# Optimization experiments

Measured on AMD Instinct MI355X. Metric: run time of the kernel, lower is better.

The kernel has to match this reference:

```python
import jax, jax.numpy as jnp
import numpy as np

N_NODES = 50000
N_EDGES = 800000
IN_DIM = 128
HID_DIM = 128
LAT_DIM = 64
NEG_SLOPE = 0.01


def _leaky(v):
    return jnp.where(v >= 0, v, NEG_SLOPE * v)


def _gcn_conv(x, W, b, src, dst, n_nodes):
    # PyG GCNConv: h = x @ W; add self-loops; sym-normalized sum aggregation; + bias
    h = x @ W  # [N, out]
    ones = jnp.ones(src.shape[0], h.dtype)
    deg = jax.ops.segment_sum(ones, dst, num_segments=n_nodes) + 1.0  # +1 self-loop
    dinv = jax.lax.rsqrt(deg)  # deg >= 1 so always finite
    norm = dinv[src] * dinv[dst]  # [E]
    agg = jax.ops.segment_sum(h[src] * norm[:, None], dst, num_segments=n_nodes)
    agg = agg + h * (dinv * dinv)[:, None]  # self-loop term: norm_ii = 1/deg_i
    return agg + b


def _glorot(key, fan_in, fan_out):
    s = jnp.sqrt(6.0 / (fan_in + fan_out)).astype(jnp.float32)
    return jax.random.uniform(key, (fan_in, fan_out), jnp.float32, -s, s)


def setup_inputs() -> dict:
    key = jax.random.key(0)
    ks = jax.random.split(key, 10)
    x = jax.random.normal(ks[0], (N_NODES, IN_DIM), jnp.float32)
    edge_index = jax.random.randint(ks[1], (2, N_EDGES), 0, N_NODES, jnp.int64)
    return {
        "x": x,
        "edge_index": edge_index,
        "W1": _glorot(ks[2], IN_DIM, HID_DIM), "b1": jnp.zeros((HID_DIM,), jnp.float32),
        "W2": _glorot(ks[3], HID_DIM, HID_DIM), "b2": jnp.zeros((HID_DIM,), jnp.float32),
        "W3": _glorot(ks[4], HID_DIM, HID_DIM), "b3": jnp.zeros((HID_DIM,), jnp.float32),
        "W4": _glorot(ks[5], HID_DIM, LAT_DIM), "b4": jnp.zeros((LAT_DIM,), jnp.float32),
        "W5": _glorot(ks[6], LAT_DIM, HID_DIM), "b5": jnp.zeros((HID_DIM,), jnp.float32),
        "Wd": _glorot(ks[7], HID_DIM, IN_DIM), "bd": jnp.zeros((IN_DIM,), jnp.float32),
    }


def reference(x, edge_index, W1, b1, W2, b2, W3, b3, W4, b4, W5, b5, Wd, bd):
    src, dst = edge_index[0], edge_index[1]
    n = x.shape[0]
    # dropout is eval-mode identity
    x1 = _leaky(_gcn_conv(x, W1, b1, src, dst, n))
    x2 = _leaky(_gcn_conv(x1, W2, b2, src, dst, n))
    x3 = _leaky(_gcn_conv(x2, W3, b3, src, dst, n)) + x2  # residual
    z = _gcn_conv(x3, W4, b4, src, dst, n)
    xr = _leaky(_gcn_conv(z, W5, b5, src, dst, n))
    reconstructed = xr @ Wd + bd + x
    return (reconstructed, z)
```

## Files before the change

### kernel.cpp

```cpp
#include <hip/hip_runtime.h>
#include <hip/hip_fp16.h>

#define NEG_SLOPE 0.01f

typedef __attribute__((ext_vector_type(4))) _Float16 half4v;
typedef __attribute__((ext_vector_type(8))) _Float16 half8v;
typedef __attribute__((ext_vector_type(4))) float f32x4;


__global__ __launch_bounds__(256) void k_count(const int* __restrict__ dst,
                                               int* __restrict__ cnt, int E) {
  int e = blockIdx.x * 256 + threadIdx.x;
  if (e < E) atomicAdd(&cnt[dst[e]], 1);
}

__global__ __launch_bounds__(256) void k_dinv(const int* __restrict__ cnt,
                                              float* __restrict__ dinv, int n) {
  int i = blockIdx.x * 256 + threadIdx.x;
  if (i < n) dinv[i] = rsqrtf((float)cnt[i] + 1.0f);
}

__global__ __launch_bounds__(256) void k_scan1(const int* __restrict__ cnt,
                                               int* __restrict__ local,
                                               int* __restrict__ bsum, int n) {
  __shared__ int lds[256];
  int b = blockIdx.x, t = threadIdx.x;
  int base = b * 1024 + t * 4;
  int v0 = (base + 0 < n) ? cnt[base + 0] : 0;
  int v1 = (base + 1 < n) ? cnt[base + 1] : 0;
  int v2 = (base + 2 < n) ? cnt[base + 2] : 0;
  int v3 = (base + 3 < n) ? cnt[base + 3] : 0;
  int s = v0 + v1 + v2 + v3;
  lds[t] = s;
  __syncthreads();
  for (int ofs = 1; ofs < 256; ofs <<= 1) {
    int x = (t >= ofs) ? lds[t - ofs] : 0;
    __syncthreads();
    lds[t] += x;
    __syncthreads();
  }
  int run = lds[t] - s;
  run += v0; if (base + 0 < n) local[base + 0] = run;
  run += v1; if (base + 1 < n) local[base + 1] = run;
  run += v2; if (base + 2 < n) local[base + 2] = run;
  run += v3; if (base + 3 < n) local[base + 3] = run;
  if (t == 255) bsum[b] = lds[255];
}

__global__ __launch_bounds__(64) void k_scan2(const int* __restrict__ bsum,
                                              int* __restrict__ bofs, int nb) {
  __shared__ int lds[64];
  int t = threadIdx.x;
  int v = (t < nb) ? bsum[t] : 0;
  lds[t] = v;
  __syncthreads();
  for (int ofs = 1; ofs < 64; ofs <<= 1) {
    int x = (t >= ofs) ? lds[t - ofs] : 0;
    __syncthreads();
    lds[t] += x;
    __syncthreads();
  }
  if (t < nb) bofs[t] = lds[t] - v;
}

__global__ __launch_bounds__(256) void k_scan3(const int* __restrict__ local,
                                               const int* __restrict__ bofs,
                                               int* __restrict__ rowptr, int n) {
  int i = blockIdx.x * 256 + threadIdx.x;
  if (i < n) rowptr[i + 1] = local[i] + bofs[i >> 10];
  if (i == 0) rowptr[0] = 0;
}

__global__ __launch_bounds__(256) void k_fill(const int* __restrict__ src,
                                              const int* __restrict__ dst,
                                              const int* __restrict__ rowptr,
                                              int* __restrict__ cursor,
                                              int2* __restrict__ slots,
                                              const float* __restrict__ dinv, int E) {
  int e = blockIdx.x * 256 + threadIdx.x;
  if (e < E) {
    int s = src[e], d = dst[e];
    int p = rowptr[d] + atomicAdd(&cursor[d], 1);
    slots[p] = make_int2(s, __float_as_int(dinv[s] * dinv[d]));
  }
}

__global__ __launch_bounds__(256) void k_wt(const float* __restrict__ W,
                                            _Float16* __restrict__ Wt, int K, int M) {
  int i = blockIdx.x * 256 + threadIdx.x;
  if (i < K * M) {
    int k = i / M, m = i % M;
    Wt[(size_t)m * K + k] = (_Float16)W[(size_t)k * M + m];
  }
}

template <int NJ>
__global__ __launch_bounds__(256) void k_hgemm(const float* __restrict__ A,
                                               const _Float16* __restrict__ Bt,
                                               float* __restrict__ C,
                                               __half* __restrict__ C16, int N, int K,
                                               int M, const float* __restrict__ bias,
                                               int leaky,
                                               const float* __restrict__ addp) {
  __shared__ _Float16 Ah[64][40];
  __shared__ _Float16 Al[64][40];
  __shared__ _Float16 Bs[NJ * 32][40];
  int t = threadIdx.x;
  int row0 = blockIdx.x * 64;
  int lane = t & 63;
  int wid = t >> 6;
  int wr = wid >> 1, wc = wid & 1;
  int l15 = lane & 15, lg = lane >> 4;
  f32x4 acc[2][NJ] = {};
  for (int k0 = 0; k0 < K; k0 += 32) {
    __syncthreads();
    for (int i = t; i < 512; i += 256) {
      int r = i >> 3, kq = i & 7;
      int gr = row0 + r;
      float4 v = make_float4(0.f, 0.f, 0.f, 0.f);
      if (gr < N) v = *(const float4*)&A[(size_t)gr * K + k0 + kq * 4];
      half4v hi = {(_Float16)v.x, (_Float16)v.y, (_Float16)v.z, (_Float16)v.w};
      half4v lo = {(_Float16)(v.x - (float)hi[0]), (_Float16)(v.y - (float)hi[1]),
                   (_Float16)(v.z - (float)hi[2]), (_Float16)(v.w - (float)hi[3])};
      *(half4v*)&Ah[r][kq * 4] = hi;
      *(half4v*)&Al[r][kq * 4] = lo;
    }
    for (int i = t; i < NJ * 32 * 4; i += 256) {
      int c = i >> 2, kg = i & 3;
      *(half8v*)&Bs[c][kg * 8] = *(const half8v*)&Bt[(size_t)c * K + k0 + kg * 8];
    }
    __syncthreads();
    half8v ah0 = *(half8v*)&Ah[wr * 32 + l15][lg * 8];
    half8v ah1 = *(half8v*)&Ah[wr * 32 + 16 + l15][lg * 8];
    half8v al0 = *(half8v*)&Al[wr * 32 + l15][lg * 8];
    half8v al1 = *(half8v*)&Al[wr * 32 + 16 + l15][lg * 8];
#pragma unroll
    for (int nj = 0; nj < NJ; ++nj) {
      half8v bf = *(half8v*)&Bs[wc * (NJ * 16) + nj * 16 + l15][lg * 8];
      acc[0][nj] = __builtin_amdgcn_mfma_f32_16x16x32_f16(ah0, bf, acc[0][nj], 0, 0, 0);
      acc[0][nj] = __builtin_amdgcn_mfma_f32_16x16x32_f16(al0, bf, acc[0][nj], 0, 0, 0);
      acc[1][nj] = __builtin_amdgcn_mfma_f32_16x16x32_f16(ah1, bf, acc[1][nj], 0, 0, 0);
      acc[1][nj] = __builtin_amdgcn_mfma_f32_16x16x32_f16(al1, bf, acc[1][nj], 0, 0, 0);
    }
  }
#pragma unroll
  for (int mi = 0; mi < 2; ++mi) {
#pragma unroll
    for (int nj = 0; nj < NJ; ++nj) {
      int c = wc * (NJ * 16) + nj * 16 + l15;
#pragma unroll
      for (int jj = 0; jj < 4; ++jj) {
        int r = row0 + wr * 32 + mi * 16 + lg * 4 + jj;
        if (r >= N) continue;
        float v = acc[mi][nj][jj];
        if (bias) v += bias[c];
        if (leaky) v = (v >= 0.f) ? v : NEG_SLOPE * v;
        if (addp) v += addp[(size_t)r * M + c];
        if (C16) C16[(size_t)r * M + c] = __float2half(v);
        else C[(size_t)r * M + c] = v;
      }
    }
  }
}

__global__ __launch_bounds__(256) void k_agg128(const __half* __restrict__ h,
                                                const int* __restrict__ rowptr,
                                                const int2* __restrict__ slots,
                                                const float* __restrict__ dinv,
                                                const float* __restrict__ bias,
                                                const float* __restrict__ resid,
                                                float* __restrict__ out, int n,
                                                int leaky) {
  int w = (blockIdx.x * 256 + threadIdx.x) >> 6;
  int lane = threadIdx.x & 63;
  if (w >= n) return;
  int beg = rowptr[w], end = rowptr[w + 1];
  float a0 = 0.f, a1 = 0.f, c0 = 0.f, c1 = 0.f;
  int j = beg;
  for (; j + 8 <= end; j += 8) {
    int2 e0 = slots[j + 0], e1 = slots[j + 1], e2 = slots[j + 2], e3 = slots[j + 3];
    int2 e4 = slots[j + 4], e5 = slots[j + 5], e6 = slots[j + 6], e7 = slots[j + 7];
    float2 h0 = __half22float2(*(const __half2*)&h[(size_t)e0.x * 128 + lane * 2]);
    float2 h1 = __half22float2(*(const __half2*)&h[(size_t)e1.x * 128 + lane * 2]);
    float2 h2 = __half22float2(*(const __half2*)&h[(size_t)e2.x * 128 + lane * 2]);
    float2 h3 = __half22float2(*(const __half2*)&h[(size_t)e3.x * 128 + lane * 2]);
    float2 h4 = __half22float2(*(const __half2*)&h[(size_t)e4.x * 128 + lane * 2]);
    float2 h5 = __half22float2(*(const __half2*)&h[(size_t)e5.x * 128 + lane * 2]);
    float2 h6 = __half22float2(*(const __half2*)&h[(size_t)e6.x * 128 + lane * 2]);
    float2 h7 = __half22float2(*(const __half2*)&h[(size_t)e7.x * 128 + lane * 2]);
    float w0 = __int_as_float(e0.y), w1 = __int_as_float(e1.y);
    float w2 = __int_as_float(e2.y), w3 = __int_as_float(e3.y);
    float w4 = __int_as_float(e4.y), w5 = __int_as_float(e5.y);
    float w6 = __int_as_float(e6.y), w7 = __int_as_float(e7.y);
    a0 += w0 * h0.x; a1 += w0 * h0.y;
    c0 += w1 * h1.x; c1 += w1 * h1.y;
    a0 += w2 * h2.x; a1 += w2 * h2.y;
    c0 += w3 * h3.x; c1 += w3 * h3.y;
    a0 += w4 * h4.x; a1 += w4 * h4.y;
    c0 += w5 * h5.x; c1 += w5 * h5.y;
    a0 += w6 * h6.x; a1 += w6 * h6.y;
    c0 += w7 * h7.x; c1 += w7 * h7.y;
  }
  for (; j < end; ++j) {
    int2 ee = slots[j];
    float wt = __int_as_float(ee.y);
    float2 hv = __half22float2(*(const __half2*)&h[(size_t)ee.x * 128 + lane * 2]);
    a0 += wt * hv.x;
    a1 += wt * hv.y;
  }
  a0 += c0; a1 += c1;
  float di = dinv[w];
  float sw = di * di;
  float2 hs = __half22float2(*(const __half2*)&h[(size_t)w * 128 + lane * 2]);
  a0 += sw * hs.x;
  a1 += sw * hs.y;
  if (bias) {
    a0 += bias[lane * 2];
    a1 += bias[lane * 2 + 1];
  }
  if (leaky) {
    a0 = (a0 >= 0.f) ? a0 : NEG_SLOPE * a0;
    a1 = (a1 >= 0.f) ? a1 : NEG_SLOPE * a1;
  }
  if (resid) {
    float2 rv = *(const float2*)&resid[(size_t)w * 128 + lane * 2];
    a0 += rv.x;
    a1 += rv.y;
  }
  *(float2*)&out[(size_t)w * 128 + lane * 2] = make_float2(a0, a1);
}

__global__ __launch_bounds__(256) void k_agg64(const __half* __restrict__ h,
                                               const int* __restrict__ rowptr,
                                               const int2* __restrict__ slots,
                                               const float* __restrict__ dinv,
                                               const float* __restrict__ bias,
                                               float* __restrict__ out,
                                               __half* __restrict__ out16, int n,
                                               int leaky) {
  int w = (blockIdx.x * 256 + threadIdx.x) >> 6;
  int lane = threadIdx.x & 63;
  if (w >= n) return;
  int beg = rowptr[w], end = rowptr[w + 1];
  float a0 = 0.f, c0 = 0.f;
  int j = beg;
  for (; j + 8 <= end; j += 8) {
    int2 e0 = slots[j + 0], e1 = slots[j + 1], e2 = slots[j + 2], e3 = slots[j + 3];
    int2 e4 = slots[j + 4], e5 = slots[j + 5], e6 = slots[j + 6], e7 = slots[j + 7];
    float h0 = __half2float(h[(size_t)e0.x * 64 + lane]);
    float h1 = __half2float(h[(size_t)e1.x * 64 + lane]);
    float h2 = __half2float(h[(size_t)e2.x * 64 + lane]);
    float h3 = __half2float(h[(size_t)e3.x * 64 + lane]);
    float h4 = __half2float(h[(size_t)e4.x * 64 + lane]);
    float h5 = __half2float(h[(size_t)e5.x * 64 + lane]);
    float h6 = __half2float(h[(size_t)e6.x * 64 + lane]);
    float h7 = __half2float(h[(size_t)e7.x * 64 + lane]);
    a0 += __int_as_float(e0.y) * h0;
    c0 += __int_as_float(e1.y) * h1;
    a0 += __int_as_float(e2.y) * h2;
    c0 += __int_as_float(e3.y) * h3;
    a0 += __int_as_float(e4.y) * h4;
    c0 += __int_as_float(e5.y) * h5;
    a0 += __int_as_float(e6.y) * h6;
    c0 += __int_as_float(e7.y) * h7;
  }
  for (; j < end; ++j) {
    int2 ee = slots[j];
    a0 += __int_as_float(ee.y) * __half2float(h[(size_t)ee.x * 64 + lane]);
  }
  a0 += c0;
  float di = dinv[w];
  a0 += di * di * __half2float(h[(size_t)w * 64 + lane]);
  if (bias) a0 += bias[lane];
  if (leaky) a0 = (a0 >= 0.f) ? a0 : NEG_SLOPE * a0;
  out[(size_t)w * 64 + lane] = a0;
  if (out16) out16[(size_t)w * 64 + lane] = __float2half(a0);
}


extern "C" void kernel_launch(void* const* d_in, const int* in_sizes, int n_in,
                              void* d_out, int out_size, void* d_ws, size_t ws_size,
                              hipStream_t stream) {
  const float* x   = (const float*)d_in[0];
  const int* eidx  = (const int*)d_in[1];
  const float* W1  = (const float*)d_in[2];
  const float* b1  = (const float*)d_in[3];
  const float* W2  = (const float*)d_in[4];
  const float* b2  = (const float*)d_in[5];
  const float* W3  = (const float*)d_in[6];
  const float* b3  = (const float*)d_in[7];
  const float* W4  = (const float*)d_in[8];
  const float* b4  = (const float*)d_in[9];
  const float* W5  = (const float*)d_in[10];
  const float* b5  = (const float*)d_in[11];
  const float* Wd  = (const float*)d_in[12];
  const float* bd  = (const float*)d_in[13];

  const int N = in_sizes[0] / 128;
  const int E = in_sizes[1] / 2;
  const int* srcA = eidx;
  const int* dstA = eidx + E;

  char* ws = (char*)d_ws;
  size_t off = 0;
  auto carve = [&](size_t bytes) {
    char* p = ws + off;
    off = (off + bytes + 255) & ~(size_t)255;
    return p;
  };
  int*   cnt      = (int*)carve((size_t)N * 4);
  int*   rowptr   = (int*)carve((size_t)(N + 1) * 4);
  int*   cursor   = (int*)carve((size_t)N * 4);
  int*   local    = (int*)carve((size_t)N * 4);
  int*   bsum     = (int*)carve(64 * 4);
  int*   bofs     = (int*)carve(64 * 4);
  float* dinv     = (float*)carve((size_t)N * 4);
  int2*  slots    = (int2*)carve((size_t)E * 8);
  float* bufA     = (float*)carve((size_t)N * 128 * 4);
  float* bufB     = (float*)carve((size_t)N * 128 * 4);
  float* bufC     = (float*)carve((size_t)N * 128 * 4);
  _Float16* Wt1   = (_Float16*)carve(128 * 128 * 2);
  _Float16* Wt2   = (_Float16*)carve(128 * 128 * 2);
  _Float16* Wt3   = (_Float16*)carve(128 * 128 * 2);
  _Float16* Wt4   = (_Float16*)carve(128 * 64 * 2);
  _Float16* Wt5   = (_Float16*)carve(64 * 128 * 2);
  _Float16* Wtd   = (_Float16*)carve(128 * 128 * 2);

  __half* h16 = (__half*)bufA;
  __half* z16 = (__half*)((char*)bufA + (size_t)N * 256);

  float* recon = (float*)d_out;
  float* zout  = (float*)d_out + (size_t)N * 128;

  const int nb = (N + 1023) / 1024;
  dim3 b256(256);

  hipMemsetAsync(cnt, 0, (size_t)N * 4, stream);
  hipMemsetAsync(cursor, 0, (size_t)N * 4, stream);
  k_count<<<(E + 255) / 256, b256, 0, stream>>>(dstA, cnt, E);
  k_dinv<<<(N + 255) / 256, b256, 0, stream>>>(cnt, dinv, N);
  k_scan1<<<nb, b256, 0, stream>>>(cnt, local, bsum, N);
  k_scan2<<<1, 64, 0, stream>>>(bsum, bofs, nb);
  k_scan3<<<(N + 255) / 256, b256, 0, stream>>>(local, bofs, rowptr, N);
  k_fill<<<(E + 255) / 256, b256, 0, stream>>>(srcA, dstA, rowptr, cursor, slots,
                                               dinv, E);

  k_wt<<<(128 * 128 + 255) / 256, b256, 0, stream>>>(W1, Wt1, 128, 128);
  k_wt<<<(128 * 128 + 255) / 256, b256, 0, stream>>>(W2, Wt2, 128, 128);
  k_wt<<<(128 * 128 + 255) / 256, b256, 0, stream>>>(W3, Wt3, 128, 128);
  k_wt<<<(128 * 64 + 255) / 256, b256, 0, stream>>>(W4, Wt4, 128, 64);
  k_wt<<<(64 * 128 + 255) / 256, b256, 0, stream>>>(W5, Wt5, 64, 128);
  k_wt<<<(128 * 128 + 255) / 256, b256, 0, stream>>>(Wd, Wtd, 128, 128);

  const int gemmBlocks = (N + 63) / 64;
  const int aggBlocks  = (N * 64 + 255) / 256;

  k_hgemm<4><<<gemmBlocks, b256, 0, stream>>>(x, Wt1, nullptr, h16, N, 128, 128,
                                              nullptr, 0, nullptr);
  k_agg128<<<aggBlocks, b256, 0, stream>>>(h16, rowptr, slots, dinv, b1, nullptr,
                                           bufB, N, 1);
  k_hgemm<4><<<gemmBlocks, b256, 0, stream>>>(bufB, Wt2, nullptr, h16, N, 128, 128,
                                              nullptr, 0, nullptr);
  k_agg128<<<aggBlocks, b256, 0, stream>>>(h16, rowptr, slots, dinv, b2, nullptr,
                                           bufC, N, 1);
  k_hgemm<4><<<gemmBlocks, b256, 0, stream>>>(bufC, Wt3, nullptr, h16, N, 128, 128,
                                              nullptr, 0, nullptr);
  k_agg128<<<aggBlocks, b256, 0, stream>>>(h16, rowptr, slots, dinv, b3, bufC,
                                           bufB, N, 1);
  k_hgemm<2><<<gemmBlocks, b256, 0, stream>>>(bufB, Wt4, nullptr, h16, N, 128, 64,
                                              nullptr, 0, nullptr);
  k_agg64<<<aggBlocks, b256, 0, stream>>>(h16, rowptr, slots, dinv, b4, zout, z16,
                                          N, 0);
  k_agg64<<<aggBlocks, b256, 0, stream>>>(z16, rowptr, slots, dinv, nullptr, bufB,
                                          nullptr, N, 0);
  k_hgemm<4><<<gemmBlocks, b256, 0, stream>>>(bufB, Wt5, bufC, nullptr, N, 64, 128,
                                              b5, 1, nullptr);
  k_hgemm<4><<<gemmBlocks, b256, 0, stream>>>(bufC, Wtd, recon, nullptr, N, 128, 128,
                                              bd, 0, x);
}
```

Before: 502.1 us.

## Split wavefront across edges with wider half4 gathers in aggregation kernels

The 128-wide and 64-wide aggregation kernels now split each wavefront into sub-groups (2 halves or 4 quarters) that handle interleaved edges. Each lane loads 8-byte half4 vectors instead of 2- or 4-byte scalars, and the partial sums are combined with cross-lane shuffles. This aims to put more independent gathers in flight per row and use wider memory transactions, which should help with average degree around 16. In exchange it adds shuffle reductions, and only a subset of lanes does the epilogue.

```diff
diff --git a/kernel.cpp b/kernel.cpp
--- a/kernel.cpp
+++ b/kernel.cpp
@@ -174,60 +174,62 @@
   int w = (blockIdx.x * 256 + threadIdx.x) >> 6;
   int lane = threadIdx.x & 63;
   if (w >= n) return;
+  int hf = lane >> 5, sl = lane & 31;
   int beg = rowptr[w], end = rowptr[w + 1];
-  float a0 = 0.f, a1 = 0.f, c0 = 0.f, c1 = 0.f;
-  int j = beg;
-  for (; j + 8 <= end; j += 8) {
-    int2 e0 = slots[j + 0], e1 = slots[j + 1], e2 = slots[j + 2], e3 = slots[j + 3];
-    int2 e4 = slots[j + 4], e5 = slots[j + 5], e6 = slots[j + 6], e7 = slots[j + 7];
-    float2 h0 = __half22float2(*(const __half2*)&h[(size_t)e0.x * 128 + lane * 2]);
-    float2 h1 = __half22float2(*(const __half2*)&h[(size_t)e1.x * 128 + lane * 2]);
-    float2 h2 = __half22float2(*(const __half2*)&h[(size_t)e2.x * 128 + lane * 2]);
-    float2 h3 = __half22float2(*(const __half2*)&h[(size_t)e3.x * 128 + lane * 2]);
-    float2 h4 = __half22float2(*(const __half2*)&h[(size_t)e4.x * 128 + lane * 2]);
-    float2 h5 = __half22float2(*(const __half2*)&h[(size_t)e5.x * 128 + lane * 2]);
-    float2 h6 = __half22float2(*(const __half2*)&h[(size_t)e6.x * 128 + lane * 2]);
-    float2 h7 = __half22float2(*(const __half2*)&h[(size_t)e7.x * 128 + lane * 2]);
+  float a0 = 0.f, a1 = 0.f, a2 = 0.f, a3 = 0.f;
+  float c0 = 0.f, c1 = 0.f, c2 = 0.f, c3 = 0.f;
+  int jj = beg + hf;
+  for (; jj + 6 < end; jj += 8) {
+    int2 e0 = slots[jj], e1 = slots[jj + 2], e2 = slots[jj + 4], e3 = slots[jj + 6];
+    half4v v0 = *(const half4v*)&h[(size_t)e0.x * 128 + sl * 4];
+    half4v v1 = *(const half4v*)&h[(size_t)e1.x * 128 + sl * 4];
+    half4v v2 = *(const half4v*)&h[(size_t)e2.x * 128 + sl * 4];
+    half4v v3 = *(const half4v*)&h[(size_t)e3.x * 128 + sl * 4];
     float w0 = __int_as_float(e0.y), w1 = __int_as_float(e1.y);
     float w2 = __int_as_float(e2.y), w3 = __int_as_float(e3.y);
-    float w4 = __int_as_float(e4.y), w5 = __int_as_float(e5.y);
-    float w6 = __int_as_float(e6.y), w7 = __int_as_float(e7.y);
-    a0 += w0 * h0.x; a1 += w0 * h0.y;
-    c0 += w1 * h1.x; c1 += w1 * h1.y;
-    a0 += w2 * h2.x; a1 += w2 * h2.y;
-    c0 += w3 * h3.x; c1 += w3 * h3.y;
-    a0 += w4 * h4.x; a1 += w4 * h4.y;
-    c0 += w5 * h5.x; c1 += w5 * h5.y;
-    a0 += w6 * h6.x; a1 += w6 * h6.y;
-    c0 += w7 * h7.x; c1 += w7 * h7.y;
-  }
-  for (; j < end; ++j) {
-    int2 ee = slots[j];
-    float wt = __int_as_float(ee.y);
-    float2 hv = __half22float2(*(const __half2*)&h[(size_t)ee.x * 128 + lane * 2]);
-    a0 += wt * hv.x;
-    a1 += wt * hv.y;
-  }
-  a0 += c0; a1 += c1;
-  float di = dinv[w];
-  float sw = di * di;
-  float2 hs = __half22float2(*(const __half2*)&h[(size_t)w * 128 + lane * 2]);
-  a0 += sw * hs.x;
-  a1 += sw * hs.y;
-  if (bias) {
-    a0 += bias[lane * 2];
-    a1 += bias[lane * 2 + 1];
-  }
-  if (leaky) {
-    a0 = (a0 >= 0.f) ? a0 : NEG_SLOPE * a0;
-    a1 = (a1 >= 0.f) ? a1 : NEG_SLOPE * a1;
-  }
-  if (resid) {
-    float2 rv = *(const float2*)&resid[(size_t)w * 128 + lane * 2];
-    a0 += rv.x;
-    a1 += rv.y;
-  }
-  *(float2*)&out[(size_t)w * 128 + lane * 2] = make_float2(a0, a1);
+    a0 += w0 * (float)v0[0]; a1 += w0 * (float)v0[1];
+    a2 += w0 * (float)v0[2]; a3 += w0 * (float)v0[3];
+    c0 += w1 * (float)v1[0]; c1 += w1 * (float)v1[1];
+    c2 += w1 * (float)v1[2]; c3 += w1 * (float)v1[3];
+    a0 += w2 * (float)v2[0]; a1 += w2 * (float)v2[1];
+    a2 += w2 * (float)v2[2]; a3 += w2 * (float)v2[3];
+    c0 += w3 * (float)v3[0]; c1 += w3 * (float)v3[1];
+    c2 += w3 * (float)v3[2]; c3 += w3 * (float)v3[3];
+  }
+  for (; jj < end; jj += 2) {
+    int2 e = slots[jj];
+    half4v v = *(const half4v*)&h[(size_t)e.x * 128 + sl * 4];
+    float wt = __int_as_float(e.y);
+    a0 += wt * (float)v[0]; a1 += wt * (float)v[1];
+    a2 += wt * (float)v[2]; a3 += wt * (float)v[3];
+  }
+  a0 += c0; a1 += c1; a2 += c2; a3 += c3;
+  a0 += __shfl_xor(a0, 32);
+  a1 += __shfl_xor(a1, 32);
+  a2 += __shfl_xor(a2, 32);
+  a3 += __shfl_xor(a3, 32);
+  if (hf == 0) {
+    float di = dinv[w];
+    float sw = di * di;
+    half4v hs = *(const half4v*)&h[(size_t)w * 128 + sl * 4];
+    a0 += sw * (float)hs[0]; a1 += sw * (float)hs[1];
+    a2 += sw * (float)hs[2]; a3 += sw * (float)hs[3];
+    if (bias) {
+      a0 += bias[sl * 4 + 0]; a1 += bias[sl * 4 + 1];
+      a2 += bias[sl * 4 + 2]; a3 += bias[sl * 4 + 3];
+    }
+    if (leaky) {
+      a0 = (a0 >= 0.f) ? a0 : NEG_SLOPE * a0;
+      a1 = (a1 >= 0.f) ? a1 : NEG_SLOPE * a1;
+      a2 = (a2 >= 0.f) ? a2 : NEG_SLOPE * a2;
+      a3 = (a3 >= 0.f) ? a3 : NEG_SLOPE * a3;
+    }
+    if (resid) {
+      float4 rv = *(const float4*)&resid[(size_t)w * 128 + sl * 4];
+      a0 += rv.x; a1 += rv.y; a2 += rv.z; a3 += rv.w;
+    }
+    *(float4*)&out[(size_t)w * 128 + sl * 4] = make_float4(a0, a1, a2, a3);
+  }
 }
 
 __global__ __launch_bounds__(256) void k_agg64(const __half* __restrict__ h,
@@ -241,40 +243,55 @@
   int w = (blockIdx.x * 256 + threadIdx.x) >> 6;
   int lane = threadIdx.x & 63;
   if (w >= n) return;
+  int q = lane >> 4, sl = lane & 15;
   int beg = rowptr[w], end = rowptr[w + 1];
-  float a0 = 0.f, c0 = 0.f;
-  int j = beg;
-  for (; j + 8 <= end; j += 8) {
-    int2 e0 = slots[j + 0], e1 = slots[j + 1], e2 = slots[j + 2], e3 = slots[j + 3];
-    int2 e4 = slots[j + 4], e5 = slots[j + 5], e6 = slots[j + 6], e7 = slots[j + 7];
-    float h0 = __half2float(h[(size_t)e0.x * 64 + lane]);
-    float h1 = __half2float(h[(size_t)e1.x * 64 + lane]);
-    float h2 = __half2float(h[(size_t)e2.x * 64 + lane]);
-    float h3 = __half2float(h[(size_t)e3.x * 64 + lane]);
-    float h4 = __half2float(h[(size_t)e4.x * 64 + lane]);
-    float h5 = __half2float(h[(size_t)e5.x * 64 + lane]);
-    float h6 = __half2float(h[(size_t)e6.x * 64 + lane]);
-    float h7 = __half2float(h[(size_t)e7.x * 64 + lane]);
-    a0 += __int_as_float(e0.y) * h0;
-    c0 += __int_as_float(e1.y) * h1;
-    a0 += __int_as_float(e2.y) * h2;
-    c0 += __int_as_float(e3.y) * h3;
-    a0 += __int_as_float(e4.y) * h4;
-    c0 += __int_as_float(e5.y) * h5;
-    a0 += __int_as_float(e6.y) * h6;
-    c0 += __int_as_float(e7.y) * h7;
-  }
-  for (; j < end; ++j) {
-    int2 ee = slots[j];
-    a0 += __int_as_float(ee.y) * __half2float(h[(size_t)ee.x * 64 + lane]);
-  }
-  a0 += c0;
-  float di = dinv[w];
-  a0 += di * di * __half2float(h[(size_t)w * 64 + lane]);
-  if (bias) a0 += bias[lane];
-  if (leaky) a0 = (a0 >= 0.f) ? a0 : NEG_SLOPE * a0;
-  out[(size_t)w * 64 + lane] = a0;
-  if (out16) out16[(size_t)w * 64 + lane] = __float2half(a0);
+  float a0 = 0.f, a1 = 0.f, a2 = 0.f, a3 = 0.f;
+  float c0 = 0.f, c1 = 0.f, c2 = 0.f, c3 = 0.f;
+  int jj = beg + q;
+  for (; jj + 4 < end; jj += 8) {
+    int2 e0 = slots[jj], e1 = slots[jj + 4];
+    half4v v0 = *(const half4v*)&h[(size_t)e0.x * 64 + sl * 4];
+    half4v v1 = *(const half4v*)&h[(size_t)e1.x * 64 + sl * 4];
+    float w0 = __int_as_float(e0.y), w1 = __int_as_float(e1.y);
+    a0 += w0 * (float)v0[0]; a1 += w0 * (float)v0[1];
+    a2 += w0 * (float)v0[2]; a3 += w0 * (float)v0[3];
+    c0 += w1 * (float)v1[0]; c1 += w1 * (float)v1[1];
+    c2 += w1 * (float)v1[2]; c3 += w1 * (float)v1[3];
+  }
+  for (; jj < end; jj += 4) {
+    int2 e = slots[jj];
+    half4v v = *(const half4v*)&h[(size_t)e.x * 64 + sl * 4];
+    float wt = __int_as_float(e.y);
+    a0 += wt * (float)v[0]; a1 += wt * (float)v[1];
+    a2 += wt * (float)v[2]; a3 += wt * (float)v[3];
+  }
+  a0 += c0; a1 += c1; a2 += c2; a3 += c3;
+  a0 += __shfl_xor(a0, 16); a0 += __shfl_xor(a0, 32);
+  a1 += __shfl_xor(a1, 16); a1 += __shfl_xor(a1, 32);
+  a2 += __shfl_xor(a2, 16); a2 += __shfl_xor(a2, 32);
+  a3 += __shfl_xor(a3, 16); a3 += __shfl_xor(a3, 32);
+  if (lane < 16) {
+    float di = dinv[w];
+    float sw = di * di;
+    half4v hs = *(const half4v*)&h[(size_t)w * 64 + sl * 4];
+    a0 += sw * (float)hs[0]; a1 += sw * (float)hs[1];
+    a2 += sw * (float)hs[2]; a3 += sw * (float)hs[3];
+    if (bias) {
+      a0 += bias[sl * 4 + 0]; a1 += bias[sl * 4 + 1];
+      a2 += bias[sl * 4 + 2]; a3 += bias[sl * 4 + 3];
+    }
+    if (leaky) {
+      a0 = (a0 >= 0.f) ? a0 : NEG_SLOPE * a0;
+      a1 = (a1 >= 0.f) ? a1 : NEG_SLOPE * a1;
+      a2 = (a2 >= 0.f) ? a2 : NEG_SLOPE * a2;
+      a3 = (a3 >= 0.f) ? a3 : NEG_SLOPE * a3;
+    }
+    *(float4*)&out[(size_t)w * 64 + sl * 4] = make_float4(a0, a1, a2, a3);
+    if (out16) {
+      half4v hv = {(_Float16)a0, (_Float16)a1, (_Float16)a2, (_Float16)a3};
+      *(half4v*)&out16[(size_t)w * 64 + sl * 4] = hv;
+    }
+  }
 }
 
 
```

Result: faster. 467.8 us (-6.8%).
